# Performance work log

Hardware: AMD Instinct MI355X
Metric: run time of the kernel (lower is better)

The kernel has to match this reference:

```python
import jax, jax.numpy as jnp
import numpy as np

B, S, HID = 2, 1024, 2048
NH, NKV, HD = 16, 4, 128
SCALE = 1.0 / np.sqrt(HD)
ROPE_BASE = 10000.0
EPS = 1e-6


def setup_inputs() -> dict:
    key = jax.random.key(0)
    ks = jax.random.split(key, 5)
    std = 0.02
    return {
        "hidden_states": jax.random.normal(ks[0], (B, S, HID), jnp.float32),
        "Wq": jax.random.normal(ks[1], (NH * HD, HID), jnp.float32) * std,
        "Wk": jax.random.normal(ks[2], (NKV * HD, HID), jnp.float32) * std,
        "Wv": jax.random.normal(ks[3], (NKV * HD, HID), jnp.float32) * std,
        "Wo": jax.random.normal(ks[4], (HID, HID), jnp.float32) * std,
        "q_norm_w": jnp.ones((HD,), jnp.float32),
        "k_norm_w": jnp.ones((HD,), jnp.float32),
    }


def _rope(x):
    # x: [B, H, S, D]; half-split rotary
    d2 = HD // 2
    inv_freq = 1.0 / (ROPE_BASE ** (jnp.arange(0, HD, 2, dtype=jnp.float32) / HD))
    ang = jnp.arange(S, dtype=jnp.float32)[:, None] * inv_freq[None, :]  # [S, d2]
    cos, sin = jnp.cos(ang), jnp.sin(ang)
    x1, x2 = x[..., :d2], x[..., d2:]
    return jnp.concatenate([x1 * cos - x2 * sin, x1 * sin + x2 * cos], axis=-1)


def _rms(x, w):
    var = jnp.mean(jnp.square(x), axis=-1, keepdims=True)
    return x * jax.lax.rsqrt(var + EPS) * w


def reference(hidden_states, Wq, Wk, Wv, Wo, q_norm_w, k_norm_w):
    b, s, _ = hidden_states.shape
    # projections (no bias)
    q = (hidden_states @ Wq.T).reshape(b, s, NH, HD).transpose(0, 2, 1, 3)
    k = (hidden_states @ Wk.T).reshape(b, s, NKV, HD).transpose(0, 2, 1, 3)
    v = (hidden_states @ Wv.T).reshape(b, s, NKV, HD).transpose(0, 2, 1, 3)
    # RoPE then per-head-dim RMS qk-norm (shared params across heads)
    q, k = _rope(q), _rope(k)
    q, k = _rms(q, q_norm_w), _rms(k, k_norm_w)
    # GQA: repeat kv heads
    groups = NH // NKV
    k = jnp.repeat(k, groups, axis=1)
    v = jnp.repeat(v, groups, axis=1)
    # stick-breaking attention, strictly causal (attend_current=False), no normalize
    logits = jnp.einsum("bhid,bhjd->bhij", q, k) * SCALE  # [B,H,S,S]
    log_p = jax.nn.log_sigmoid(logits)
    log_om = jax.nn.log_sigmoid(-logits)  # log(1 - p)
    i = jnp.arange(s)
    mask = i[None, :] < i[:, None]  # j < i
    masked_om = jnp.where(mask, log_om, 0.0)
    # cum[i,j] = sum_{j < k < i} log(1-p[i,k]) : exclusive reversed cumsum
    cum = jnp.flip(jnp.cumsum(jnp.flip(masked_om, -1), -1), -1) - masked_om
    att = jnp.where(mask, jnp.exp(log_p + cum), 0.0)
    o = jnp.einsum("bhij,bhjd->bhid", att, v)
    o = o.transpose(0, 2, 1, 3).reshape(b, s, NH * HD)
    return o @ Wo.T
```

## Files before the change

kernel.cpp:

```cpp
#include <hip/hip_runtime.h>
#include <math.h>

#define B_    2
#define S_    1024
#define HID_  2048
#define NH_   16
#define NKV_  4
#define HD_   128
#define GROUPS (NH_ / NKV_)
#define SCALE_ 0.08838834764831845f

#define NZ_   4
#define QPSZ  4194304
#define KPSZ  1048576

typedef _Float16 f16x8 __attribute__((ext_vector_type(8)));
typedef _Float16 f16x4 __attribute__((ext_vector_type(4)));
typedef float    f32x4 __attribute__((ext_vector_type(4)));

__device__ __forceinline__ void async_copy16(const void* g, void* l) {
    __builtin_amdgcn_global_load_lds(
        (const __attribute__((address_space(1))) void*)g,
        (__attribute__((address_space(3))) void*)l, 16, 0, 0);
}

__device__ __forceinline__ int dpp_swap1(int x) {
    return __builtin_amdgcn_update_dpp(0, x, 0xB1, 0xF, 0xF, true);
}

__global__ __launch_bounds__(256) void cast5_f16(
    const float4* __restrict__ s0, ushort4* __restrict__ d0, int n0,
    const float4* __restrict__ s1, ushort4* __restrict__ d1, int n1,
    const float4* __restrict__ s2, ushort4* __restrict__ d2, int n2,
    const float4* __restrict__ s3, ushort4* __restrict__ d3, int n3,
    const float4* __restrict__ s4, ushort4* __restrict__ d4, int n4)
{
    int i = blockIdx.x * 256 + threadIdx.x;
    const float4* s; ushort4* d; int idx;
    if (i < n0)                          { s = s0; d = d0; idx = i; }
    else if (i < n0 + n1)                { s = s1; d = d1; idx = i - n0; }
    else if (i < n0 + n1 + n2)           { s = s2; d = d2; idx = i - n0 - n1; }
    else if (i < n0 + n1 + n2 + n3)      { s = s3; d = d3; idx = i - n0 - n1 - n2; }
    else if (i < n0 + n1 + n2 + n3 + n4) { s = s4; d = d4; idx = i - n0 - n1 - n2 - n3; }
    else return;
    float4 v = s[idx];
    _Float16 a = (_Float16)v.x, b = (_Float16)v.y,
             c = (_Float16)v.z, e = (_Float16)v.w;
    ushort4 o;
    o.x = *(unsigned short*)&a; o.y = *(unsigned short*)&b;
    o.z = *(unsigned short*)&c; o.w = *(unsigned short*)&e;
    d[idx] = o;
}

__global__ __launch_bounds__(256) void qkv_gemm(
    const _Float16* __restrict__ A,
    const _Float16* __restrict__ Wq,
    const _Float16* __restrict__ Wk,
    const _Float16* __restrict__ Wv,
    _Float16* __restrict__ Qp,
    _Float16* __restrict__ Kp,
    _Float16* __restrict__ Vp)
{
    __shared__ __align__(16) unsigned char smem[32768];

    const int tid  = threadIdx.x;
    const int lane = tid & 63, wave = tid >> 6;
    const int wr = (wave >> 1) * 64, wc = (wave & 1) * 64;
    const int bm = blockIdx.y * 128;
    const int bt = blockIdx.x;
    const int z  = blockIdx.z;
    const int kbase = z * (HID_ / NZ_);

    const _Float16* Wsel;
    _Float16* Csel;
    int nrow0, heads;
    if (bt < 16)      { Wsel = Wq; Csel = Qp + (size_t)z * QPSZ; nrow0 = bt * 128;        heads = NH_;  }
    else if (bt < 20) { Wsel = Wk; Csel = Kp + (size_t)z * KPSZ; nrow0 = (bt - 16) * 128; heads = NKV_; }
    else              { Wsel = Wv; Csel = Vp + (size_t)z * KPSZ; nrow0 = (bt - 20) * 128; heads = NKV_; }

    const int srow = 32 * wave + (lane >> 2);
    const int scol = (lane & 3) * 8;
    const _Float16* Ag = A    + (size_t)(bm + srow)    * HID_ + kbase + scol;
    const _Float16* Wg = Wsel + (size_t)(nrow0 + srow) * HID_ + kbase + scol;

    const unsigned aoff = (unsigned)(wave * 2048);

    f32x4 acc[4][4];
    const f32x4 fz = {0.f, 0.f, 0.f, 0.f};
#pragma unroll
    for (int i = 0; i < 4; i++)
#pragma unroll
        for (int j = 0; j < 4; j++) acc[i][j] = fz;

    const int ml = lane & 15, kg = lane >> 4;

#define QKV_STAGE(d, k0) do {                                                 \
        _Float16* la_ = (_Float16*)(smem + (d) * 16384 + aoff);               \
        _Float16* lw_ = (_Float16*)(smem + (d) * 16384 + 8192 + aoff);        \
        async_copy16(Ag + (k0), la_);                                         \
        async_copy16(Ag + (k0) + (size_t)16 * HID_, la_ + 16 * 32);           \
        async_copy16(Wg + (k0), lw_);                                         \
        async_copy16(Wg + (k0) + (size_t)16 * HID_, lw_ + 16 * 32);           \
    } while (0)

    QKV_STAGE(0, 0);
    __syncthreads();

    int d = 0;
    for (int t = 0; t < 16; t++) {
        if (t < 15) QKV_STAGE(d ^ 1, (t + 1) * 32);

        const _Float16* tA = (const _Float16*)(smem + d * 16384);
        const _Float16* tW = (const _Float16*)(smem + d * 16384 + 8192);

        f16x8 a[4], b[4];
#pragma unroll
        for (int mi = 0; mi < 4; mi++)
            a[mi] = *(const f16x8*)&tA[(wr + mi * 16 + ml) * 32 + kg * 8];
#pragma unroll
        for (int ni = 0; ni < 4; ni++)
            b[ni] = *(const f16x8*)&tW[(wc + ni * 16 + ml) * 32 + kg * 8];
#pragma unroll
        for (int mi = 0; mi < 4; mi++)
#pragma unroll
            for (int ni = 0; ni < 4; ni++)
                acc[mi][ni] = __builtin_amdgcn_mfma_f32_16x16x32_f16(
                    a[mi], b[ni], acc[mi][ni], 0, 0, 0);

        __syncthreads();
        d ^= 1;
    }
#undef QKV_STAGE

#pragma unroll
    for (int mi = 0; mi < 4; mi++) {
#pragma unroll
        for (int ni = 0; ni < 4; ni++) {
#pragma unroll
            for (int r = 0; r < 4; r++) {
                int m = bm + wr + mi * 16 + kg * 4 + r;
                int n = nrow0 + wc + ni * 16 + ml;
                int hh = n >> 7, d2 = n & 127;
                int b_ = m >> 10, s = m & 1023;
                size_t idx = (((size_t)(b_ * heads + hh)) * S_ + s) * HD_ + d2;
                Csel[idx] = (_Float16)acc[mi][ni][r];
            }
        }
    }
}

__global__ __launch_bounds__(512) void out_gemm(
    const _Float16* __restrict__ A,
    const _Float16* __restrict__ W,
    float* __restrict__ Cout)
{
    __shared__ __align__(16) unsigned char smem[66560];

    const int tid  = threadIdx.x;
    const int lane = tid & 63, wave = tid >> 6;
    const int kh = wave >> 2;
    const int wv = wave & 3;
    const int wr = (wv >> 1) * 64, wc = (wv & 1) * 64;
    const int bm = blockIdx.y * 128, bn = blockIdx.x * 128;
    const int kbase = kh * (HID_ / 2);

    const int srow = 32 * wv + (lane >> 2);
    const int scol = (lane & 3) * 8;
    const _Float16* Ag = A + (size_t)(bm + srow) * HID_ + kbase + scol;
    const _Float16* Wg = W + (size_t)(bn + srow) * HID_ + kbase + scol;

    const unsigned aoff = (unsigned)(kh * 8192 + 32 * wv * 64);
    const unsigned woff = (unsigned)(16384 + kh * 8192 + 32 * wv * 64);

    f32x4 acc[4][4];
    const f32x4 fz = {0.f, 0.f, 0.f, 0.f};
#pragma unroll
    for (int i = 0; i < 4; i++)
#pragma unroll
        for (int j = 0; j < 4; j++) acc[i][j] = fz;

    const int ml = lane & 15, kg = lane >> 4;

#define OG_STAGE(d, k0) do {                                                  \
        _Float16* la_ = (_Float16*)(smem + (d) * 32768 + aoff);               \
        _Float16* lw_ = (_Float16*)(smem + (d) * 32768 + woff);               \
        async_copy16(Ag + (k0), la_);                                         \
        async_copy16(Ag + (k0) + (size_t)16 * HID_, la_ + 16 * 32);           \
        async_copy16(Wg + (k0), lw_);                                         \
        async_copy16(Wg + (k0) + (size_t)16 * HID_, lw_ + 16 * 32);           \
    } while (0)

#define OG_COMPUTE(d) do {                                                    \
        const _Float16* tA = (const _Float16*)(smem + (d) * 32768 + kh * 8192);\
        const _Float16* tW = (const _Float16*)(smem + (d) * 32768 + 16384 + kh * 8192);\
        f16x8 a[4], b[4];                                                     \
        _Pragma("unroll")                                                     \
        for (int mi = 0; mi < 4; mi++)                                        \
            a[mi] = *(const f16x8*)&tA[(wr + mi * 16 + ml) * 32 + kg * 8];    \
        _Pragma("unroll")                                                     \
        for (int ni = 0; ni < 4; ni++)                                        \
            b[ni] = *(const f16x8*)&tW[(wc + ni * 16 + ml) * 32 + kg * 8];    \
        _Pragma("unroll")                                                     \
        for (int mi = 0; mi < 4; mi++)                                        \
            _Pragma("unroll")                                                 \
            for (int ni = 0; ni < 4; ni++)                                    \
                acc[mi][ni] = __builtin_amdgcn_mfma_f32_16x16x32_f16(         \
                    a[mi], b[ni], acc[mi][ni], 0, 0, 0);                      \
    } while (0)

    OG_STAGE(0, 0);
    asm volatile("s_waitcnt vmcnt(0)" ::: "memory");
    __builtin_amdgcn_s_barrier();

    int d = 0;
    for (int t = 0; t < 31; t++) {
        OG_STAGE(d ^ 1, (t + 1) * 32);
        asm volatile("s_waitcnt vmcnt(4)" ::: "memory");
        __builtin_amdgcn_s_barrier();
        __builtin_amdgcn_sched_barrier(0);

        OG_COMPUTE(d);

        __builtin_amdgcn_sched_barrier(0);
        __builtin_amdgcn_s_barrier();
        d ^= 1;
    }
    asm volatile("s_waitcnt vmcnt(0)" ::: "memory");
    __builtin_amdgcn_s_barrier();
    __builtin_amdgcn_sched_barrier(0);
    OG_COMPUTE(d);
#undef OG_STAGE
#undef OG_COMPUTE

    __syncthreads();
    float* red = (float*)smem;
    float* rp  = red + ((size_t)(wv * 64 + lane)) * 65;
    if (kh == 1) {
#pragma unroll
        for (int mi = 0; mi < 4; mi++)
#pragma unroll
            for (int ni = 0; ni < 4; ni++)
#pragma unroll
                for (int r = 0; r < 4; r++)
                    rp[mi * 16 + ni * 4 + r] = acc[mi][ni][r];
    }
    __syncthreads();
    if (kh == 0) {
#pragma unroll
        for (int mi = 0; mi < 4; mi++)
#pragma unroll
            for (int ni = 0; ni < 4; ni++)
#pragma unroll
                for (int r = 0; r < 4; r++) {
                    float v = acc[mi][ni][r] + rp[mi * 16 + ni * 4 + r];
                    int m = bm + wr + mi * 16 + kg * 4 + r;
                    int n = bn + wc + ni * 16 + ml;
                    Cout[(size_t)m * HID_ + n] = v;
                }
    }
}

__global__ __launch_bounds__(256) void rope_rms_v(
    const _Float16* __restrict__ Qp, const _Float16* __restrict__ Kp,
    const _Float16* __restrict__ Vp,
    const float* __restrict__ qw, const float* __restrict__ kw,
    _Float16* __restrict__ Qout, _Float16* __restrict__ Kout,
    _Float16* __restrict__ Vout)
{
    int row = blockIdx.x * 4 + (threadIdx.x >> 6);
    int lane = threadIdx.x & 63;

    if (row >= 40960) {
        int lrow = row - 40960;
        size_t off = (size_t)lrow * HD_ + lane * 2;
        float a0 = 0.f, a1 = 0.f;
#pragma unroll
        for (int zp = 0; zp < NZ_; zp++) {
            a0 += (float)Vp[(size_t)zp * KPSZ + off];
            a1 += (float)Vp[(size_t)zp * KPSZ + off + 1];
        }
        _Float16* q = Vout + (size_t)lrow * HD_;
        q[lane * 2]     = (_Float16)a0;
        q[lane * 2 + 1] = (_Float16)a1;
        return;
    }

    bool isQ = row < 32768;
    int lrow = isQ ? row : row - 32768;
    const _Float16* p0 = isQ ? Qp : Kp;
    size_t psz = isQ ? QPSZ : KPSZ;
    _Float16* q = (isQ ? Qout : Kout) + (size_t)lrow * HD_;
    const float* w = isQ ? qw : kw;
    int s = row & (S_ - 1);

    size_t base = (size_t)lrow * HD_;
    float x1 = 0.f, x2 = 0.f;
#pragma unroll
    for (int zp = 0; zp < NZ_; zp++) {
        x1 += (float)p0[(size_t)zp * psz + base + lane];
        x2 += (float)p0[(size_t)zp * psz + base + lane + 64];
    }

    float invf = __builtin_amdgcn_exp2f(-(float)lane * 0.2076205059304601f);
    float ang = (float)s * invf;
    float sn = __sinf(ang);
    float c  = __cosf(ang);

    float y1 = x1 * c - x2 * sn;
    float y2 = x1 * sn + x2 * c;

    float ss = y1 * y1 + y2 * y2;
#pragma unroll
    for (int off = 32; off > 0; off >>= 1) ss += __shfl_xor(ss, off);

    float scl = rsqrtf(ss * (1.0f / 128.0f) + 1e-6f);
    q[lane]      = (_Float16)(y1 * scl * w[lane]);
    q[lane + 64] = (_Float16)(y2 * scl * w[lane + 64]);
}

#define QK_STR 136
#define VT_STR 72
#define SS_STR 68
#define AT_STR 72

__global__ __launch_bounds__(512) void stick_attn(
    const _Float16* __restrict__ Q, const _Float16* __restrict__ K,
    const _Float16* __restrict__ V, _Float16* __restrict__ AO)
{
    __shared__ __align__(16) _Float16 Qs[64][QK_STR];
    __shared__ __align__(16) _Float16 Ks[64][QK_STR];
    __shared__ __align__(16) _Float16 Vt[128][VT_STR];
    __shared__ __align__(16) float    Ss[64][SS_STR];
    __shared__ __align__(16) _Float16 atts[64][AT_STR];
    __shared__ float paccs[64];

    const int bid = blockIdx.x;
    const int slot = bid & 255, phase = bid >> 8;
    const int hb = slot >> 3, iw = slot & 7;
    const int b = hb >> 4, h = hb & 15;
    const int qb = phase ? iw : 15 - iw;

    const int kvh = h / GROUPS;
    const int tid = threadIdx.x;
    const int lane = tid & 63, wave = tid >> 6;
    const int qw = wave >> 1;
    const int kh = wave & 1;
    const int ml = lane & 15, quad = lane >> 4;

    const _Float16* Kbase = K + ((size_t)(b * NKV_ + kvh) * S_) * HD_;
    const _Float16* Vbase = V + ((size_t)(b * NKV_ + kvh) * S_) * HD_;

    const f32x4 fz = {0.f, 0.f, 0.f, 0.f};

    const int qi0 = qb * 64;
    const _Float16* Qbase = Q + ((size_t)(b * NH_ + h) * S_ + qi0) * HD_;

    const int kr = tid >> 4, kc = (tid & 15) * 8;
    const _Float16* Vrow = Vbase + (size_t)lane * HD_ + wave * 16;

    f16x8 kA, kB, vA, vB;
    {
        const _Float16* kp = Kbase + (size_t)(qb * 64 + kr) * HD_ + kc;
        kA = *(const f16x8*)(kp);
        kB = *(const f16x8*)(kp + (size_t)32 * HD_);
        const _Float16* vp = Vrow + (size_t)(qb * 64) * HD_;
        vA = *(const f16x8*)(vp);
        vB = *(const f16x8*)(vp + 8);
    }

    for (int idx = tid; idx < 64 * 16; idx += 512) {
        int r = idx >> 4, c8 = (idx & 15) * 8;
        *(f16x8*)&Qs[r][c8] = *(const f16x8*)(Qbase + r * HD_ + c8);
    }
    if (tid < 64) paccs[tid] = 1.f;
    __syncthreads();

    f16x8 aq[4];
#pragma unroll
    for (int ks = 0; ks < 4; ks++)
        aq[ks] = *(const f16x8*)&Qs[qw * 16 + ml][ks * 32 + quad * 8];

    f32x4 accO[4] = {fz, fz, fz, fz};

    for (int kb = qb; kb >= 0; --kb) {
        __syncthreads();

        *(f16x8*)&Ks[kr][kc]      = kA;
        *(f16x8*)&Ks[kr + 32][kc] = kB;

        {
            int4 i0 = *(int4*)&vA, i1 = *(int4*)&vB;
            int4 p0, p1;
            p0.x = dpp_swap1(i0.x); p0.y = dpp_swap1(i0.y);
            p0.z = dpp_swap1(i0.z); p0.w = dpp_swap1(i0.w);
            p1.x = dpp_swap1(i1.x); p1.y = dpp_swap1(i1.y);
            p1.z = dpp_swap1(i1.z); p1.w = dpp_swap1(i1.w);
            bool ev = !(lane & 1);
            int4 al = ev ? i0 : p1;
            int4 bh = ev ? p0 : i1;
            int r0w = wave * 16 + (ev ? 0 : 8);
            int colk = lane & ~1;
            int ac[4] = {al.x, al.y, al.z, al.w};
            int bc[4] = {bh.x, bh.y, bh.z, bh.w};
#pragma unroll
            for (int i = 0; i < 8; i++) {
                int c = i >> 1;
                unsigned pack = (i & 1)
                    ? (((unsigned)ac[c] >> 16) | ((unsigned)bc[c] & 0xffff0000u))
                    : (((unsigned)ac[c] & 0xffffu) | ((unsigned)bc[c] << 16));
                *(unsigned*)&Vt[r0w + i][colk] = pack;
            }
        }
        __syncthreads();

        if (kb > 0) {
            const _Float16* kp = Kbase + (size_t)((kb - 1) * 64 + kr) * HD_ + kc;
            kA = *(const f16x8*)(kp);
            kB = *(const f16x8*)(kp + (size_t)32 * HD_);
            const _Float16* vp = Vrow + (size_t)((kb - 1) * 64) * HD_;
            vA = *(const f16x8*)(vp);
            vB = *(const f16x8*)(vp + 8);
        }

        f32x4 accS[2] = {fz, fz};
        __builtin_amdgcn_s_setprio(1);
#pragma unroll
        for (int ks = 0; ks < 4; ks++) {
#pragma unroll
            for (int ni = 0; ni < 2; ni++) {
                f16x8 bf = *(const f16x8*)
                    &Ks[kh * 32 + ni * 16 + ml][ks * 32 + quad * 8];
                accS[ni] = __builtin_amdgcn_mfma_f32_16x16x32_f16(
                    aq[ks], bf, accS[ni], 0, 0, 0);
            }
        }
        __builtin_amdgcn_s_setprio(0);
#pragma unroll
        for (int ni = 0; ni < 2; ni++)
#pragma unroll
            for (int r = 0; r < 4; r++)
                Ss[qw * 16 + quad * 4 + r][kh * 32 + ni * 16 + ml] =
                    accS[ni][r] * SCALE_;
        __syncthreads();

        {
            int q = tid >> 3, seg = tid & 7;
            int qg = qi0 + q;
            int j0 = kb * 64 + seg * 8;
            float4 s0 = *(float4*)&Ss[q][seg * 8];
            float4 s1 = *(float4*)&Ss[q][seg * 8 + 4];
            float L[8] = {s0.x, s0.y, s0.z, s0.w, s1.x, s1.y, s1.z, s1.w};
            float sv[8], om[8];
#pragma unroll
            for (int i = 0; i < 8; i++) {
                float u = __expf(L[i]);
                float o = __builtin_amdgcn_rcpf(1.f + u);
                bool valid = (j0 + i < qg);
                om[i] = valid ? o : 1.f;
                sv[i] = valid ? (1.f - o) : 0.f;
            }
            float suf = 1.f, lo[8];
#pragma unroll
            for (int i = 7; i >= 0; --i) {
                lo[i] = suf; suf *= om[i];
            }
            float x = suf;
#pragma unroll
            for (int off = 1; off < 8; off <<= 1) {
                float y = __shfl_down(x, off);
                if (seg + off < 8) x *= y;
            }
            float bx = __shfl_down(x, 1);
            float base = (seg == 7) ? 1.f : bx;
            float paccq = paccs[q];
            float pb = base * paccq;
            f16x8 av;
#pragma unroll
            for (int i = 0; i < 8; i++)
                av[i] = (_Float16)(sv[i] * lo[i] * pb);
            *(f16x8*)&atts[q][seg * 8] = av;
            if (seg == 0) paccs[q] = paccq * x;
        }
        __syncthreads();

        __builtin_amdgcn_s_setprio(1);
#pragma unroll
        for (int ks = 0; ks < 2; ks++) {
            f16x8 ap = *(const f16x8*)&atts[qw * 16 + ml][ks * 32 + quad * 8];
#pragma unroll
            for (int ni = 0; ni < 4; ni++) {
                f16x8 bv = *(const f16x8*)
                    &Vt[kh * 64 + ni * 16 + ml][ks * 32 + quad * 8];
                accO[ni] = __builtin_amdgcn_mfma_f32_16x16x32_f16(
                    ap, bv, accO[ni], 0, 0, 0);
            }
        }
        __builtin_amdgcn_s_setprio(0);
    }

#pragma unroll
    for (int ni = 0; ni < 4; ni++) {
#pragma unroll
        for (int r = 0; r < 4; r++) {
            int qg = qi0 + qw * 16 + quad * 4 + r;
            int d = kh * 64 + ni * 16 + ml;
            AO[((size_t)(b * S_ + qg) * NH_ + h) * HD_ + d] =
                (_Float16)accO[ni][r];
        }
    }
}

extern "C" void kernel_launch(void* const* d_in, const int* in_sizes, int n_in,
                              void* d_out, int out_size, void* d_ws, size_t ws_size,
                              hipStream_t stream)
{
    const float* hs = (const float*)d_in[0];
    const float* Wq = (const float*)d_in[1];
    const float* Wk = (const float*)d_in[2];
    const float* Wv = (const float*)d_in[3];
    const float* Wo = (const float*)d_in[4];
    const float* qw = (const float*)d_in[5];
    const float* kw = (const float*)d_in[6];
    float* out = (float*)d_out;

    _Float16* Qp  = (_Float16*)d_ws;
    _Float16* Kp  = Qp + (size_t)NZ_ * QPSZ;
    _Float16* Vp  = Kp + (size_t)NZ_ * KPSZ;
    _Float16* hsh = Vp + (size_t)NZ_ * KPSZ;
    _Float16* Wqh = hsh + 4194304;
    _Float16* Wkh = Wqh + 4194304;
    _Float16* Wvh = Wkh + 1048576;
    _Float16* Woh = Wvh + 1048576;
    _Float16* Qh  = Woh + 4194304;
    _Float16* Kh  = Qh + 4194304;
    _Float16* Vh  = Kh + 1048576;
    _Float16* AOh = hsh;

    dim3 blk(256);

    cast5_f16<<<14336, blk, 0, stream>>>(
        (const float4*)hs, (ushort4*)hsh, 1048576,
        (const float4*)Wq, (ushort4*)Wqh, 1048576,
        (const float4*)Wk, (ushort4*)Wkh, 262144,
        (const float4*)Wv, (ushort4*)Wvh, 262144,
        (const float4*)Wo, (ushort4*)Woh, 1048576);

    qkv_gemm<<<dim3(24, 16, NZ_), blk, 0, stream>>>(hsh, Wqh, Wkh, Wvh,
                                                    Qp, Kp, Vp);

    rope_rms_v<<<dim3(49152 / 4), blk, 0, stream>>>(
        Qp, Kp, Vp, qw, kw, Qh, Kh, Vh);

    stick_attn<<<dim3(512), dim3(512), 0, stream>>>(Qh, Kh, Vh, AOh);

    out_gemm<<<dim3(16, 16), dim3(512), 0, stream>>>(AOh, Woh, out);
}
```

Before: 211.9 us.

## Halve QKV split-K factor and pipeline LDS loads with explicit vmcnt waits

```diff
diff --git a/kernel.cpp b/kernel.cpp
--- a/kernel.cpp
+++ b/kernel.cpp
@@ -10,7 +10,7 @@
 #define GROUPS (NH_ / NKV_)
 #define SCALE_ 0.08838834764831845f
 
-#define NZ_   4
+#define NZ_   2
 #define QPSZ  4194304
 #define KPSZ  1048576
 
@@ -103,34 +103,47 @@
         async_copy16(Wg + (k0) + (size_t)16 * HID_, lw_ + 16 * 32);           \
     } while (0)
 
+#define QKV_COMPUTE(d) do {                                                   \
+        const _Float16* tA = (const _Float16*)(smem + (d) * 16384);           \
+        const _Float16* tW = (const _Float16*)(smem + (d) * 16384 + 8192);    \
+        f16x8 a[4], b[4];                                                     \
+        _Pragma("unroll")                                                     \
+        for (int mi = 0; mi < 4; mi++)                                        \
+            a[mi] = *(const f16x8*)&tA[(wr + mi * 16 + ml) * 32 + kg * 8];    \
+        _Pragma("unroll")                                                     \
+        for (int ni = 0; ni < 4; ni++)                                        \
+            b[ni] = *(const f16x8*)&tW[(wc + ni * 16 + ml) * 32 + kg * 8];    \
+        _Pragma("unroll")                                                     \
+        for (int mi = 0; mi < 4; mi++)                                        \
+            _Pragma("unroll")                                                 \
+            for (int ni = 0; ni < 4; ni++)                                    \
+                acc[mi][ni] = __builtin_amdgcn_mfma_f32_16x16x32_f16(         \
+                    a[mi], b[ni], acc[mi][ni], 0, 0, 0);                      \
+    } while (0)
+
     QKV_STAGE(0, 0);
-    __syncthreads();
+    asm volatile("s_waitcnt vmcnt(0)" ::: "memory");
+    __builtin_amdgcn_s_barrier();
 
     int d = 0;
-    for (int t = 0; t < 16; t++) {
-        if (t < 15) QKV_STAGE(d ^ 1, (t + 1) * 32);
-
-        const _Float16* tA = (const _Float16*)(smem + d * 16384);
-        const _Float16* tW = (const _Float16*)(smem + d * 16384 + 8192);
-
-        f16x8 a[4], b[4];
-#pragma unroll
-        for (int mi = 0; mi < 4; mi++)
-            a[mi] = *(const f16x8*)&tA[(wr + mi * 16 + ml) * 32 + kg * 8];
-#pragma unroll
-        for (int ni = 0; ni < 4; ni++)
-            b[ni] = *(const f16x8*)&tW[(wc + ni * 16 + ml) * 32 + kg * 8];
-#pragma unroll
-        for (int mi = 0; mi < 4; mi++)
-#pragma unroll
-            for (int ni = 0; ni < 4; ni++)
-                acc[mi][ni] = __builtin_amdgcn_mfma_f32_16x16x32_f16(
-                    a[mi], b[ni], acc[mi][ni], 0, 0, 0);
-
-        __syncthreads();
+    for (int t = 0; t < 31; t++) {
+        QKV_STAGE(d ^ 1, (t + 1) * 32);
+        asm volatile("s_waitcnt vmcnt(4)" ::: "memory");
+        __builtin_amdgcn_s_barrier();
+        __builtin_amdgcn_sched_barrier(0);
+
+        QKV_COMPUTE(d);
+
+        __builtin_amdgcn_sched_barrier(0);
+        __builtin_amdgcn_s_barrier();
         d ^= 1;
     }
+    asm volatile("s_waitcnt vmcnt(0)" ::: "memory");
+    __builtin_amdgcn_s_barrier();
+    __builtin_amdgcn_sched_barrier(0);
+    QKV_COMPUTE(d);
 #undef QKV_STAGE
+#undef QKV_COMPUTE
 
 #pragma unroll
     for (int mi = 0; mi < 4; mi++) {
```

After: 208.9 us. No clear change (-1.4%).
